# Kernel tuning notes

Measured on AMD Instinct MI355X. Metric: run time of the kernel, lower is better.

Reference implementation:

```python
import jax, jax.numpy as jnp
import numpy as np

B, T, D, H = 4, 2048, 1024, 16
DH = D // H


def setup_inputs() -> dict:
    key = jax.random.key(0)
    ks = jax.random.split(key, 7)
    s = 1.0 / np.sqrt(D)
    inp = {
        "query": jax.random.normal(ks[0], (B, T, D), jnp.float32),
        "key": jax.random.normal(ks[1], (B, T, D), jnp.float32),
        "value": jax.random.normal(ks[2], (B, T, D), jnp.float32),
        "wq": jax.random.normal(ks[3], (D, D), jnp.float32) * s,
        "wk": jax.random.normal(ks[4], (D, D), jnp.float32) * s,
        "wv": jax.random.normal(ks[5], (D, D), jnp.float32) * s,
        "wo": jax.random.normal(ks[6], (D, D), jnp.float32) * s,
    }
    # additive causal mask, broadcast over batch and heads
    neg = jnp.finfo(jnp.float32).min
    causal = jnp.where(jnp.tril(jnp.ones((T, T), bool)), 0.0, neg)
    inp["attn_mask"] = causal[None, None, :, :].astype(jnp.float32)
    return inp


def _split_heads(x):
    # [B, T, D] -> [B, H, T, DH]
    Bx, Tx, _ = x.shape
    return x.reshape(Bx, Tx, H, DH).transpose(0, 2, 1, 3)


def reference(query, key, value, attn_mask, wq, wk, wv, wo):
    # nn.Linear(bias=False): y = x @ W^T
    q = _split_heads(query @ wq.T)
    k = _split_heads(key @ wk.T)
    v = _split_heads(value @ wv.T)
    scale = 1.0 / jnp.sqrt(jnp.asarray(DH, q.dtype))
    scores = jnp.einsum("bhqd,bhkd->bhqk", q, k) * scale + attn_mask
    weights = jax.nn.softmax(scores, axis=-1)
    out = jnp.einsum("bhqk,bhkd->bhqd", weights, v)
    out = out.transpose(0, 2, 1, 3).reshape(query.shape[0], query.shape[1], D)
    out = out @ wo.T
    return out, k, v
```

## Files before the change

### kernel.cpp

```cpp
#include <hip/hip_runtime.h>
#include <hip/hip_bf16.h>
#include <math.h>

constexpr int Mdim = 8192;
constexpr int Ndim = 1024;
constexpr int Kdim = 1024;
constexpr int Tseq = 2048;
constexpr int NH   = 16;

typedef __attribute__((ext_vector_type(8))) short short8;
typedef __attribute__((ext_vector_type(4))) float floatx4;

__device__ __forceinline__ unsigned short f2b(float f) {
  unsigned int x = __builtin_bit_cast(unsigned int, f);
  x += 0x7fffu + ((x >> 16) & 1u);
  return (unsigned short)(x >> 16);
}
__device__ __forceinline__ unsigned int pk2(float a, float b) {
  unsigned int ua = __builtin_bit_cast(unsigned int, a) + 0x8000u;
  unsigned int ub = __builtin_bit_cast(unsigned int, b) + 0x8000u;
  return (ua >> 16) | (ub & 0xffff0000u);
}
__device__ __forceinline__ void gld16(const void* g, const void* l) {
  __builtin_amdgcn_global_load_lds(
      (const __attribute__((address_space(1))) unsigned int*)(unsigned long long)g,
      (__attribute__((address_space(3))) unsigned int*)(unsigned int)(unsigned long long)l,
      16, 0, 0);
}
__device__ __forceinline__ void barrier_raw() {
  __builtin_amdgcn_sched_barrier(0);
  __builtin_amdgcn_s_barrier();
  __builtin_amdgcn_sched_barrier(0);
}

__global__ __launch_bounds__(256) void cast_k(
    const float* __restrict__ q, const float* __restrict__ k,
    const float* __restrict__ v, const float* __restrict__ wq,
    const float* __restrict__ wk, const float* __restrict__ wv,
    const float* __restrict__ wo,
    unsigned short* d0, unsigned short* d1, unsigned short* d2,
    unsigned short* d3, unsigned short* d4, unsigned short* d5,
    unsigned short* d6) {
  int y = blockIdx.y;
  const float* s = y == 0 ? q : y == 1 ? k : y == 2 ? v
                 : y == 3 ? wq : y == 4 ? wk : y == 5 ? wv : wo;
  unsigned short* d = y == 0 ? d0 : y == 1 ? d1 : y == 2 ? d2
                    : y == 3 ? d3 : y == 4 ? d4 : y == 5 ? d5 : d6;
  size_t n = (y < 3) ? (size_t)Mdim * Kdim : (size_t)Ndim * Kdim;
  size_t i = ((size_t)blockIdx.x * 256 + threadIdx.x) * 8;
  if (i >= n) return;
  float4 a = *(const float4*)(s + i);
  float4 b = *(const float4*)(s + i + 4);
  uint4 w;
  w.x = (unsigned)f2b(a.x) | ((unsigned)f2b(a.y) << 16);
  w.y = (unsigned)f2b(a.z) | ((unsigned)f2b(a.w) << 16);
  w.z = (unsigned)f2b(b.x) | ((unsigned)f2b(b.y) << 16);
  w.w = (unsigned)f2b(b.z) | ((unsigned)f2b(b.w) << 16);
  *(uint4*)(d + i) = w;
}

__launch_bounds__(256, 4)
__global__ void gemm_qkv(const unsigned short* __restrict__ Aq,
                         const unsigned short* __restrict__ Ak,
                         const unsigned short* __restrict__ Av,
                         const unsigned short* __restrict__ Wq,
                         const unsigned short* __restrict__ Wk,
                         const unsigned short* __restrict__ Wv,
                         unsigned short* __restrict__ Qh,
                         unsigned short* __restrict__ Kh,
                         float* __restrict__ Kout,
                         unsigned short* __restrict__ VTg,
                         float* __restrict__ Vout) {
  __shared__ __align__(16) unsigned short As[128 * 64];
  __shared__ __align__(16) unsigned short Bs[128 * 64];

  const int flat = (blockIdx.z * 64 + blockIdx.y) * 8 + blockIdx.x;
  const int wgid = (flat & 7) * 192 + (flat >> 3);
  const int z    = wgid >> 9;
  const int rem  = wgid & 511;
  const int m0   = (rem >> 3) * 128;
  const int n0   = (rem & 7) * 128;

  const unsigned short* __restrict__ A = z == 0 ? Aq : z == 1 ? Ak : Av;
  const unsigned short* __restrict__ W = z == 0 ? Wq : z == 1 ? Wk : Wv;

  const int tid  = threadIdx.x;
  const int lane = tid & 63;
  const int wave = tid >> 6;
  const int l15  = lane & 15;
  const int quad = lane >> 4;
  const int sw   = l15 & 7;
  const int wm = (wave >> 1) * 64;
  const int wn = (wave & 1) * 64;

  floatx4 acc[4][4];
  for (int i = 0; i < 4; i++)
    for (int j = 0; j < 4; j++) acc[i][j] = (floatx4)0.0f;

  const int srow8 = lane >> 3;
  const int sg    = lane & 7;

  for (int kt = 0; kt < Kdim; kt += 64) {
    for (int jj = 0; jj < 4; jj++) {
      int cc = wave * 4 + jj;
      int row = cc * 8 + srow8;
      int G = sg ^ (row & 7);
      gld16(A + (size_t)(m0 + row) * Kdim + kt + G * 8, As + cc * 512);
      gld16(W + (size_t)(n0 + row) * Kdim + kt + G * 8, Bs + cc * 512);
    }
    __syncthreads();

    for (int hf = 0; hf < 2; hf++) {
      short8 af[4], bw[4];
      for (int mi = 0; mi < 4; mi++)
        af[mi] = *(const short8*)(As + (wm + mi * 16 + l15) * 64 +
                                  (((hf * 4 + quad) ^ sw) << 3));
      for (int ni = 0; ni < 4; ni++)
        bw[ni] = *(const short8*)(Bs + (wn + ni * 16 + l15) * 64 +
                                  (((hf * 4 + quad) ^ sw) << 3));
      for (int mi = 0; mi < 4; mi++)
        for (int ni = 0; ni < 4; ni++)
          acc[mi][ni] = __builtin_amdgcn_mfma_f32_16x16x32_bf16(
              bw[ni], af[mi], acc[mi][ni], 0, 0, 0);
    }
    __syncthreads();
  }

  const int gm = m0 + wm + l15;
  for (int mi = 0; mi < 4; mi++) {
    int t_abs = gm + mi * 16;
    int b = t_abs >> 11, tb = t_abs & (Tseq - 1);
    for (int ni = 0; ni < 4; ni++) {
      int gn0 = n0 + wn + ni * 16 + quad * 4;
      int h = gn0 >> 6, dh0 = gn0 & 63;
      size_t base = ((size_t)((b * NH + h) * Tseq + tb)) * 64 + dh0;
      floatx4 v = acc[mi][ni];
      if (z == 0) {
        ushort4 w = {f2b(v[0]), f2b(v[1]), f2b(v[2]), f2b(v[3])};
        *(ushort4*)(Qh + base) = w;
      } else if (z == 1) {
        *(float4*)(Kout + base) = *(float4*)&v;
        ushort4 w = {f2b(v[0]), f2b(v[1]), f2b(v[2]), f2b(v[3])};
        *(ushort4*)(Kh + base) = w;
      } else {
        *(float4*)(Vout + base) = *(float4*)&v;
        size_t vtb = ((size_t)((b * NH + h) * 64 + dh0)) * Tseq + tb;
        for (int r = 0; r < 4; r++)
          VTg[vtb + (size_t)r * Tseq] = f2b(v[r]);
      }
    }
  }
}

__launch_bounds__(256)
__global__ void gemm_o(const unsigned short* __restrict__ A,
                       const unsigned short* __restrict__ W,
                       float* __restrict__ Cf) {
  __shared__ __align__(16) unsigned short As[128 * 64];
  __shared__ __align__(16) unsigned short Bs[128 * 64];

  const int tid  = threadIdx.x;
  const int lane = tid & 63;
  const int wave = tid >> 6;
  const int l15  = lane & 15;
  const int quad = lane >> 4;
  const int sw   = l15 & 7;
  const int m0 = blockIdx.y * 128;
  const int n0 = blockIdx.x * 128;
  const int wm = (wave >> 1) * 64;
  const int wn = (wave & 1) * 64;

  floatx4 acc[4][4];
  for (int i = 0; i < 4; i++)
    for (int j = 0; j < 4; j++) acc[i][j] = (floatx4)0.0f;

  const int srow8 = lane >> 3;
  const int sg    = lane & 7;

  for (int kt = 0; kt < Kdim; kt += 64) {
    for (int jj = 0; jj < 4; jj++) {
      int cc = wave * 4 + jj;
      int row = cc * 8 + srow8;
      int G = sg ^ (row & 7);
      gld16(A + (size_t)(m0 + row) * Kdim + kt + G * 8, As + cc * 512);
      gld16(W + (size_t)(n0 + row) * Kdim + kt + G * 8, Bs + cc * 512);
    }
    __syncthreads();

    for (int hf = 0; hf < 2; hf++) {
      short8 af[4], bw[4];
      for (int mi = 0; mi < 4; mi++)
        af[mi] = *(const short8*)(As + (wm + mi * 16 + l15) * 64 +
                                  (((hf * 4 + quad) ^ sw) << 3));
      for (int ni = 0; ni < 4; ni++)
        bw[ni] = *(const short8*)(Bs + (wn + ni * 16 + l15) * 64 +
                                  (((hf * 4 + quad) ^ sw) << 3));
      for (int mi = 0; mi < 4; mi++)
        for (int ni = 0; ni < 4; ni++)
          acc[mi][ni] = __builtin_amdgcn_mfma_f32_16x16x32_bf16(
              bw[ni], af[mi], acc[mi][ni], 0, 0, 0);
    }
    __syncthreads();
  }

  for (int mi = 0; mi < 4; mi++) {
    int t_abs = m0 + wm + mi * 16 + l15;
    for (int ni = 0; ni < 4; ni++) {
      int gn0 = n0 + wn + ni * 16 + quad * 4;
      floatx4 v = acc[mi][ni];
      *(float4*)(Cf + (size_t)t_abs * Ndim + gn0) = *(float4*)&v;
    }
  }
}

__launch_bounds__(256)
__global__ void attn_k(const unsigned short* __restrict__ Qh,
                       const unsigned short* __restrict__ Kh,
                       const unsigned short* __restrict__ VTg,
                       unsigned short* __restrict__ Og) {
  __shared__ __align__(16) unsigned short Kt[2][64 * 64];
  __shared__ __align__(16) unsigned short Vt[2][64 * 64];
  __shared__ __align__(16) unsigned short Pl[64 * 64];

  const int tid  = threadIdx.x;
  const int lane = tid & 63;
  const int wave = tid >> 6;
  const int l15  = lane & 15;
  const int quad = lane >> 4;
  const int sw   = l15 & 7;
  const int bh   = blockIdx.x;

  const size_t headoff = (size_t)bh * Tseq * 64;
  const int srow8 = lane >> 3;
  const int sg    = lane & 7;
  const float kscale = 0.18033688011112042f;
  const int b = bh >> 4, h = bh & 15;

  for (int half = 0; half < 2; half++) {
    const int a   = half ? blockIdx.y : 31 - blockIdx.y;
    const int nkt = a + 1;
    const int qg  = a * 64 + wave * 16 + l15;

    short8 bq[2];
#pragma unroll
    for (int hf = 0; hf < 2; hf++)
      bq[hf] = *(const short8*)(Qh + headoff + (size_t)qg * 64 +
                                hf * 32 + quad * 8);

    floatx4 o[4];
#pragma unroll
    for (int nb = 0; nb < 4; nb++) o[nb] = (floatx4)0.0f;
    float mrow = -INFINITY, lrow = 0.0f;

    auto stage = [&](int par, int kt) {
      const int k0 = kt * 64;
#pragma unroll
      for (int jj = 0; jj < 2; jj++) {
        int cc  = wave * 2 + jj;
        int row = cc * 8 + srow8;
        int G   = sg ^ (row & 7);
        gld16(Kh + headoff + (size_t)(k0 + row) * 64 + G * 8,
              &Kt[par][cc * 512]);
        gld16(VTg + ((size_t)bh * 64 + row) * Tseq + k0 + G * 8,
              &Vt[par][cc * 512]);
      }
    };

    stage(0, 0);
    __builtin_amdgcn_sched_barrier(0);
    asm volatile("s_waitcnt vmcnt(0)");
    barrier_raw();

    for (int kt = 0; kt < nkt; kt++) {
      const int par = kt & 1;
      if (kt + 1 < nkt) stage(par ^ 1, kt + 1);
      const int k0 = kt * 64;

      floatx4 st[4];
#pragma unroll
      for (int nb = 0; nb < 4; nb++) {
        const unsigned short* kr = &Kt[par][(nb * 16 + l15) * 64];
        short8 ak0 = *(const short8*)(kr + ((quad ^ sw) << 3));
        short8 ak1 = *(const short8*)(kr + (((quad + 4) ^ sw) << 3));
        floatx4 acc0 = (floatx4)0.0f;
        acc0 = __builtin_amdgcn_mfma_f32_16x16x32_bf16(ak0, bq[0], acc0, 0, 0, 0);
        acc0 = __builtin_amdgcn_mfma_f32_16x16x32_bf16(ak1, bq[1], acc0, 0, 0, 0);
        st[nb] = acc0;
      }

      if (kt == nkt - 1) {
#pragma unroll
        for (int nb = 0; nb < 4; nb++)
#pragma unroll
          for (int r = 0; r < 4; r++) {
            int kg = k0 + nb * 16 + quad * 4 + r;
            if (kg > qg) st[nb][r] = -INFINITY;
          }
      }

      float mt = fmaxf(fmaxf(st[0][0], st[0][1]), fmaxf(st[0][2], st[0][3]));
#pragma unroll
      for (int nb = 1; nb < 4; nb++)
        mt = fmaxf(mt, fmaxf(fmaxf(st[nb][0], st[nb][1]),
                             fmaxf(st[nb][2], st[nb][3])));
      mt = fmaxf(mt, __shfl_xor(mt, 16, 64));
      mt = fmaxf(mt, __shfl_xor(mt, 32, 64));

      if (!__all((mt - mrow) * kscale <= 8.0f)) {
        float mnew = fmaxf(mrow, mt);
        float al = __builtin_amdgcn_exp2f((mrow - mnew) * kscale);
        mrow = mnew;
        lrow *= al;
#pragma unroll
        for (int nb = 0; nb < 4; nb++)
#pragma unroll
          for (int r = 0; r < 4; r++) o[nb][r] *= al;
      }
      const float ms = mrow * kscale;

      float rs = 0.0f;
      const int prow = (wave * 16 + l15) * 64;
#pragma unroll
      for (int nb = 0; nb < 4; nb++) {
        float p0 = __builtin_amdgcn_exp2f(__builtin_fmaf(st[nb][0], kscale, -ms));
        float p1 = __builtin_amdgcn_exp2f(__builtin_fmaf(st[nb][1], kscale, -ms));
        float p2 = __builtin_amdgcn_exp2f(__builtin_fmaf(st[nb][2], kscale, -ms));
        float p3 = __builtin_amdgcn_exp2f(__builtin_fmaf(st[nb][3], kscale, -ms));
        rs += (p0 + p1) + (p2 + p3);
        uint2 w = {pk2(p0, p1), pk2(p2, p3)};
        int klb = nb * 16 + quad * 4;
        int colp = (((klb >> 3) ^ sw) << 3) | (klb & 7);
        *(uint2*)(Pl + prow + colp) = w;
      }
      rs += __shfl_xor(rs, 16, 64);
      rs += __shfl_xor(rs, 32, 64);
      lrow += rs;

      short8 av[4][2];
#pragma unroll
      for (int nb = 0; nb < 4; nb++) {
        const unsigned short* vr = &Vt[par][(nb * 16 + l15) * 64];
        av[nb][0] = *(const short8*)(vr + ((quad ^ sw) << 3));
        av[nb][1] = *(const short8*)(vr + (((quad + 4) ^ sw) << 3));
      }
      const unsigned short* pr = Pl + prow;
      short8 bp0 = *(const short8*)(pr + ((quad ^ sw) << 3));
      short8 bp1 = *(const short8*)(pr + (((quad + 4) ^ sw) << 3));
#pragma unroll
      for (int nb = 0; nb < 4; nb++) {
        o[nb] = __builtin_amdgcn_mfma_f32_16x16x32_bf16(av[nb][0], bp0, o[nb], 0, 0, 0);
        o[nb] = __builtin_amdgcn_mfma_f32_16x16x32_bf16(av[nb][1], bp1, o[nb], 0, 0, 0);
      }

      __builtin_amdgcn_sched_barrier(0);
      asm volatile("s_waitcnt vmcnt(0)");
      barrier_raw();
    }

    float inv = 1.0f / lrow;
    size_t rowoff = ((size_t)(b * Tseq + qg)) * 1024 + h * 64;
#pragma unroll
    for (int nb = 0; nb < 4; nb++) {
      ushort4 w;
      w.x = f2b(o[nb][0] * inv);
      w.y = f2b(o[nb][1] * inv);
      w.z = f2b(o[nb][2] * inv);
      w.w = f2b(o[nb][3] * inv);
      *(ushort4*)(Og + rowoff + nb * 16 + quad * 4) = w;
    }
  }
}

extern "C" void kernel_launch(void* const* d_in, const int* in_sizes, int n_in,
                              void* d_out, int out_size, void* d_ws, size_t ws_size,
                              hipStream_t stream) {
  const float* q  = (const float*)d_in[0];
  const float* k  = (const float*)d_in[1];
  const float* v  = (const float*)d_in[2];
  const float* wq = (const float*)d_in[3];
  const float* wk = (const float*)d_in[4];
  const float* wv = (const float*)d_in[5];
  const float* wo = (const float*)d_in[6];
  float* out = (float*)d_out;

  constexpr size_t BTD = (size_t)Mdim * Kdim;
  constexpr size_t DD  = (size_t)Ndim * Kdim;
  constexpr size_t MB16 = BTD * 2;

  char* ws = (char*)d_ws;
  unsigned short* Qh  = (unsigned short*)(ws);
  unsigned short* Kh  = (unsigned short*)(ws + MB16);
  unsigned short* VTg = (unsigned short*)(ws + 2 * MB16);
  unsigned short* Og  = (unsigned short*)(ws + 3 * MB16);
  unsigned short* qb  = (unsigned short*)(ws + 4 * MB16);
  unsigned short* kb  = (unsigned short*)(ws + 5 * MB16);
  unsigned short* vb  = (unsigned short*)(ws + 6 * MB16);
  unsigned short* wqb = (unsigned short*)(ws + 7 * MB16);
  unsigned short* wkb = wqb + DD;
  unsigned short* wvb = wkb + DD;
  unsigned short* wob = wvb + DD;

  float* Kout = out + BTD;
  float* Vout = out + 2 * BTD;

  cast_k<<<dim3(4096, 7), 256, 0, stream>>>(q, k, v, wq, wk, wv, wo,
                                            qb, kb, vb, wqb, wkb, wvb, wob);

  gemm_qkv<<<dim3(8, 64, 3), 256, 0, stream>>>(
      qb, kb, vb, wqb, wkb, wvb, Qh, Kh, Kout, VTg, Vout);

  attn_k<<<dim3(4 * NH, 16), 256, 0, stream>>>(Qh, Kh, VTg, Og);

  gemm_o<<<dim3(Ndim / 128, Mdim / 128), 256, 0, stream>>>(Og, wob, out);
}
```

Measured before the change: 366.2 us.

## Retile output GEMM, split attention blocks per query tile, single-buffer V

The attention kernel now launches one block per 64-row query tile instead of pairing two tiles per block, and keeps only a single V buffer in shared memory. V is loaded in the same iteration it is used, with a mid-iteration wait before the PV product. Packed bf16 conversion and a three-input max instruction replace manual bit tricks and pairwise maxes. The output GEMM uses 64x128 tiles with a grouped block ordering and occupancy hints, which doubles the block count and shrinks shared memory per block. Together these aim to raise occupancy and parallelism, at the cost of losing the causal load balancing from pairing and exposing V load latency.

```diff
diff --git a/kernel.cpp b/kernel.cpp
--- a/kernel.cpp
+++ b/kernel.cpp
@@ -16,10 +16,15 @@
   x += 0x7fffu + ((x >> 16) & 1u);
   return (unsigned short)(x >> 16);
 }
-__device__ __forceinline__ unsigned int pk2(float a, float b) {
-  unsigned int ua = __builtin_bit_cast(unsigned int, a) + 0x8000u;
-  unsigned int ub = __builtin_bit_cast(unsigned int, b) + 0x8000u;
-  return (ua >> 16) | (ub & 0xffff0000u);
+__device__ __forceinline__ unsigned int cvtpk(float a, float b) {
+  unsigned int r;
+  asm("v_cvt_pk_bf16_f32 %0, %1, %2" : "=v"(r) : "v"(a), "v"(b));
+  return r;
+}
+__device__ __forceinline__ float max3f(float a, float b, float c) {
+  float d;
+  asm("v_max3_f32 %0, %1, %2, %3" : "=v"(d) : "v"(a), "v"(b), "v"(c));
+  return d;
 }
 __device__ __forceinline__ void gld16(const void* g, const void* l) {
   __builtin_amdgcn_global_load_lds(
@@ -152,12 +157,17 @@
   }
 }
 
-__launch_bounds__(256)
+__launch_bounds__(256, 6)
 __global__ void gemm_o(const unsigned short* __restrict__ A,
                        const unsigned short* __restrict__ W,
                        float* __restrict__ Cf) {
-  __shared__ __align__(16) unsigned short As[128 * 64];
+  __shared__ __align__(16) unsigned short As[64 * 64];
   __shared__ __align__(16) unsigned short Bs[128 * 64];
+
+  const int flat = blockIdx.y * 8 + blockIdx.x;
+  const int wgid = (flat & 7) * 128 + (flat >> 3);
+  const int m0   = (wgid >> 3) * 64;
+  const int n0   = (wgid & 7) * 128;
 
   const int tid  = threadIdx.x;
   const int lane = tid & 63;
@@ -165,37 +175,40 @@
   const int l15  = lane & 15;
   const int quad = lane >> 4;
   const int sw   = l15 & 7;
-  const int m0 = blockIdx.y * 128;
-  const int n0 = blockIdx.x * 128;
-  const int wm = (wave >> 1) * 64;
+  const int wm = (wave >> 1) * 32;
   const int wn = (wave & 1) * 64;
 
-  floatx4 acc[4][4];
-  for (int i = 0; i < 4; i++)
+  floatx4 acc[2][4];
+  for (int i = 0; i < 2; i++)
     for (int j = 0; j < 4; j++) acc[i][j] = (floatx4)0.0f;
 
   const int srow8 = lane >> 3;
   const int sg    = lane & 7;
 
   for (int kt = 0; kt < Kdim; kt += 64) {
+    for (int jj = 0; jj < 2; jj++) {
+      int cc = wave * 2 + jj;
+      int row = cc * 8 + srow8;
+      int G = sg ^ (row & 7);
+      gld16(A + (size_t)(m0 + row) * Kdim + kt + G * 8, As + cc * 512);
+    }
     for (int jj = 0; jj < 4; jj++) {
       int cc = wave * 4 + jj;
       int row = cc * 8 + srow8;
       int G = sg ^ (row & 7);
-      gld16(A + (size_t)(m0 + row) * Kdim + kt + G * 8, As + cc * 512);
       gld16(W + (size_t)(n0 + row) * Kdim + kt + G * 8, Bs + cc * 512);
     }
     __syncthreads();
 
     for (int hf = 0; hf < 2; hf++) {
-      short8 af[4], bw[4];
-      for (int mi = 0; mi < 4; mi++)
+      short8 af[2], bw[4];
+      for (int mi = 0; mi < 2; mi++)
         af[mi] = *(const short8*)(As + (wm + mi * 16 + l15) * 64 +
                                   (((hf * 4 + quad) ^ sw) << 3));
       for (int ni = 0; ni < 4; ni++)
         bw[ni] = *(const short8*)(Bs + (wn + ni * 16 + l15) * 64 +
                                   (((hf * 4 + quad) ^ sw) << 3));
-      for (int mi = 0; mi < 4; mi++)
+      for (int mi = 0; mi < 2; mi++)
         for (int ni = 0; ni < 4; ni++)
           acc[mi][ni] = __builtin_amdgcn_mfma_f32_16x16x32_bf16(
               bw[ni], af[mi], acc[mi][ni], 0, 0, 0);
@@ -203,7 +216,7 @@
     __syncthreads();
   }
 
-  for (int mi = 0; mi < 4; mi++) {
+  for (int mi = 0; mi < 2; mi++) {
     int t_abs = m0 + wm + mi * 16 + l15;
     for (int ni = 0; ni < 4; ni++) {
       int gn0 = n0 + wn + ni * 16 + quad * 4;
@@ -213,13 +226,13 @@
   }
 }
 
-__launch_bounds__(256)
+__launch_bounds__(256, 5)
 __global__ void attn_k(const unsigned short* __restrict__ Qh,
                        const unsigned short* __restrict__ Kh,
                        const unsigned short* __restrict__ VTg,
                        unsigned short* __restrict__ Og) {
   __shared__ __align__(16) unsigned short Kt[2][64 * 64];
-  __shared__ __align__(16) unsigned short Vt[2][64 * 64];
+  __shared__ __align__(16) unsigned short Vt[64 * 64];
   __shared__ __align__(16) unsigned short Pl[64 * 64];
 
   const int tid  = threadIdx.x;
@@ -229,145 +242,158 @@
   const int quad = lane >> 4;
   const int sw   = l15 & 7;
   const int bh   = blockIdx.x;
+  const int a    = 31 - (int)blockIdx.y;
+  const int nkt  = a + 1;
 
   const size_t headoff = (size_t)bh * Tseq * 64;
   const int srow8 = lane >> 3;
   const int sg    = lane & 7;
   const float kscale = 0.18033688011112042f;
   const int b = bh >> 4, h = bh & 15;
-
-  for (int half = 0; half < 2; half++) {
-    const int a   = half ? blockIdx.y : 31 - blockIdx.y;
-    const int nkt = a + 1;
-    const int qg  = a * 64 + wave * 16 + l15;
-
-    short8 bq[2];
-#pragma unroll
-    for (int hf = 0; hf < 2; hf++)
-      bq[hf] = *(const short8*)(Qh + headoff + (size_t)qg * 64 +
-                                hf * 32 + quad * 8);
-
-    floatx4 o[4];
-#pragma unroll
-    for (int nb = 0; nb < 4; nb++) o[nb] = (floatx4)0.0f;
-    float mrow = -INFINITY, lrow = 0.0f;
-
-    auto stage = [&](int par, int kt) {
-      const int k0 = kt * 64;
-#pragma unroll
-      for (int jj = 0; jj < 2; jj++) {
-        int cc  = wave * 2 + jj;
-        int row = cc * 8 + srow8;
-        int G   = sg ^ (row & 7);
-        gld16(Kh + headoff + (size_t)(k0 + row) * 64 + G * 8,
-              &Kt[par][cc * 512]);
-        gld16(VTg + ((size_t)bh * 64 + row) * Tseq + k0 + G * 8,
-              &Vt[par][cc * 512]);
-      }
-    };
-
-    stage(0, 0);
+  const int qg = a * 64 + wave * 16 + l15;
+
+  short8 bq[2];
+#pragma unroll
+  for (int hf = 0; hf < 2; hf++)
+    bq[hf] = *(const short8*)(Qh + headoff + (size_t)qg * 64 +
+                              hf * 32 + quad * 8);
+
+  floatx4 o[4];
+#pragma unroll
+  for (int nb = 0; nb < 4; nb++) o[nb] = (floatx4)0.0f;
+  float mrow = -INFINITY, lrow = 0.0f;
+
+  auto stageK = [&](int par, int kt) {
+    const int k0 = kt * 64;
+#pragma unroll
+    for (int jj = 0; jj < 2; jj++) {
+      int cc  = wave * 2 + jj;
+      int row = cc * 8 + srow8;
+      int G   = sg ^ (row & 7);
+      gld16(Kh + headoff + (size_t)(k0 + row) * 64 + G * 8, &Kt[par][cc * 512]);
+    }
+  };
+  auto stageV = [&](int kt) {
+    const int k0 = kt * 64;
+#pragma unroll
+    for (int jj = 0; jj < 2; jj++) {
+      int cc  = wave * 2 + jj;
+      int row = cc * 8 + srow8;
+      int G   = sg ^ (row & 7);
+      gld16(VTg + ((size_t)bh * 64 + row) * Tseq + k0 + G * 8, Vt + cc * 512);
+    }
+  };
+
+  stageK(0, 0);
+  __builtin_amdgcn_sched_barrier(0);
+  asm volatile("s_waitcnt vmcnt(0)");
+  barrier_raw();
+
+  for (int kt = 0; kt < nkt; kt++) {
+    const int par = kt & 1;
+    const int k0 = kt * 64;
+    stageV(kt);
+    const bool pre = (kt + 1 < nkt);
+    if (pre) stageK(par ^ 1, kt + 1);
+    __builtin_amdgcn_sched_barrier(0);
+
+    floatx4 st[4];
+#pragma unroll
+    for (int nb = 0; nb < 4; nb++) {
+      const unsigned short* kr = &Kt[par][(nb * 16 + l15) * 64];
+      short8 ak0 = *(const short8*)(kr + ((quad ^ sw) << 3));
+      short8 ak1 = *(const short8*)(kr + (((quad + 4) ^ sw) << 3));
+      floatx4 acc0 = (floatx4)0.0f;
+      acc0 = __builtin_amdgcn_mfma_f32_16x16x32_bf16(ak0, bq[0], acc0, 0, 0, 0);
+      acc0 = __builtin_amdgcn_mfma_f32_16x16x32_bf16(ak1, bq[1], acc0, 0, 0, 0);
+      st[nb] = acc0;
+    }
+
+    if (kt == nkt - 1) {
+#pragma unroll
+      for (int nb = 0; nb < 4; nb++)
+#pragma unroll
+        for (int r = 0; r < 4; r++) {
+          int kg = k0 + nb * 16 + quad * 4 + r;
+          if (kg > qg) st[nb][r] = -INFINITY;
+        }
+    }
+
+    float m0_ = max3f(st[0][0], st[0][1], st[0][2]);
+    float m1_ = max3f(st[0][3], st[1][0], st[1][1]);
+    float m2_ = max3f(st[1][2], st[1][3], st[2][0]);
+    float m3_ = max3f(st[2][1], st[2][2], st[2][3]);
+    float m4_ = max3f(st[3][0], st[3][1], st[3][2]);
+    float mt = fmaxf(max3f(m0_, m1_, m2_), max3f(m3_, m4_, st[3][3]));
+    mt = fmaxf(mt, __shfl_xor(mt, 16, 64));
+    mt = fmaxf(mt, __shfl_xor(mt, 32, 64));
+
+    if (!__all((mt - mrow) * kscale <= 8.0f)) {
+      float mnew = fmaxf(mrow, mt);
+      float al = __builtin_amdgcn_exp2f((mrow - mnew) * kscale);
+      mrow = mnew;
+      lrow *= al;
+#pragma unroll
+      for (int nb = 0; nb < 4; nb++)
+#pragma unroll
+        for (int r = 0; r < 4; r++) o[nb][r] *= al;
+    }
+    const float ms = mrow * kscale;
+
+    float rs = 0.0f;
+    const int prow = (wave * 16 + l15) * 64;
+#pragma unroll
+    for (int nb = 0; nb < 4; nb++) {
+      float p0 = __builtin_amdgcn_exp2f(__builtin_fmaf(st[nb][0], kscale, -ms));
+      float p1 = __builtin_amdgcn_exp2f(__builtin_fmaf(st[nb][1], kscale, -ms));
+      float p2 = __builtin_amdgcn_exp2f(__builtin_fmaf(st[nb][2], kscale, -ms));
+      float p3 = __builtin_amdgcn_exp2f(__builtin_fmaf(st[nb][3], kscale, -ms));
+      rs += (p0 + p1) + (p2 + p3);
+      uint2 w = {cvtpk(p0, p1), cvtpk(p2, p3)};
+      int klb = nb * 16 + quad * 4;
+      int colp = (((klb >> 3) ^ sw) << 3) | (klb & 7);
+      *(uint2*)(Pl + prow + colp) = w;
+    }
+    rs += __shfl_xor(rs, 16, 64);
+    rs += __shfl_xor(rs, 32, 64);
+    lrow += rs;
+
+    __builtin_amdgcn_sched_barrier(0);
+    if (pre) asm volatile("s_waitcnt vmcnt(2)");
+    else     asm volatile("s_waitcnt vmcnt(0)");
+    barrier_raw();
+
+    short8 av[4][2];
+#pragma unroll
+    for (int nb = 0; nb < 4; nb++) {
+      const unsigned short* vr = Vt + (nb * 16 + l15) * 64;
+      av[nb][0] = *(const short8*)(vr + ((quad ^ sw) << 3));
+      av[nb][1] = *(const short8*)(vr + (((quad + 4) ^ sw) << 3));
+    }
+    const unsigned short* pr = Pl + prow;
+    short8 bp0 = *(const short8*)(pr + ((quad ^ sw) << 3));
+    short8 bp1 = *(const short8*)(pr + (((quad + 4) ^ sw) << 3));
+#pragma unroll
+    for (int nb = 0; nb < 4; nb++) {
+      o[nb] = __builtin_amdgcn_mfma_f32_16x16x32_bf16(av[nb][0], bp0, o[nb], 0, 0, 0);
+      o[nb] = __builtin_amdgcn_mfma_f32_16x16x32_bf16(av[nb][1], bp1, o[nb], 0, 0, 0);
+    }
+
     __builtin_amdgcn_sched_barrier(0);
     asm volatile("s_waitcnt vmcnt(0)");
     barrier_raw();
-
-    for (int kt = 0; kt < nkt; kt++) {
-      const int par = kt & 1;
-      if (kt + 1 < nkt) stage(par ^ 1, kt + 1);
-      const int k0 = kt * 64;
-
-      floatx4 st[4];
-#pragma unroll
-      for (int nb = 0; nb < 4; nb++) {
-        const unsigned short* kr = &Kt[par][(nb * 16 + l15) * 64];
-        short8 ak0 = *(const short8*)(kr + ((quad ^ sw) << 3));
-        short8 ak1 = *(const short8*)(kr + (((quad + 4) ^ sw) << 3));
-        floatx4 acc0 = (floatx4)0.0f;
-        acc0 = __builtin_amdgcn_mfma_f32_16x16x32_bf16(ak0, bq[0], acc0, 0, 0, 0);
-        acc0 = __builtin_amdgcn_mfma_f32_16x16x32_bf16(ak1, bq[1], acc0, 0, 0, 0);
-        st[nb] = acc0;
-      }
-
-      if (kt == nkt - 1) {
-#pragma unroll
-        for (int nb = 0; nb < 4; nb++)
-#pragma unroll
-          for (int r = 0; r < 4; r++) {
-            int kg = k0 + nb * 16 + quad * 4 + r;
-            if (kg > qg) st[nb][r] = -INFINITY;
-          }
-      }
-
-      float mt = fmaxf(fmaxf(st[0][0], st[0][1]), fmaxf(st[0][2], st[0][3]));
-#pragma unroll
-      for (int nb = 1; nb < 4; nb++)
-        mt = fmaxf(mt, fmaxf(fmaxf(st[nb][0], st[nb][1]),
-                             fmaxf(st[nb][2], st[nb][3])));
-      mt = fmaxf(mt, __shfl_xor(mt, 16, 64));
-      mt = fmaxf(mt, __shfl_xor(mt, 32, 64));
-
-      if (!__all((mt - mrow) * kscale <= 8.0f)) {
-        float mnew = fmaxf(mrow, mt);
-        float al = __builtin_amdgcn_exp2f((mrow - mnew) * kscale);
-        mrow = mnew;
-        lrow *= al;
-#pragma unroll
-        for (int nb = 0; nb < 4; nb++)
-#pragma unroll
-          for (int r = 0; r < 4; r++) o[nb][r] *= al;
-      }
-      const float ms = mrow * kscale;
-
-      float rs = 0.0f;
-      const int prow = (wave * 16 + l15) * 64;
-#pragma unroll
-      for (int nb = 0; nb < 4; nb++) {
-        float p0 = __builtin_amdgcn_exp2f(__builtin_fmaf(st[nb][0], kscale, -ms));
-        float p1 = __builtin_amdgcn_exp2f(__builtin_fmaf(st[nb][1], kscale, -ms));
-        float p2 = __builtin_amdgcn_exp2f(__builtin_fmaf(st[nb][2], kscale, -ms));
-        float p3 = __builtin_amdgcn_exp2f(__builtin_fmaf(st[nb][3], kscale, -ms));
-        rs += (p0 + p1) + (p2 + p3);
-        uint2 w = {pk2(p0, p1), pk2(p2, p3)};
-        int klb = nb * 16 + quad * 4;
-        int colp = (((klb >> 3) ^ sw) << 3) | (klb & 7);
-        *(uint2*)(Pl + prow + colp) = w;
-      }
-      rs += __shfl_xor(rs, 16, 64);
-      rs += __shfl_xor(rs, 32, 64);
-      lrow += rs;
-
-      short8 av[4][2];
-#pragma unroll
-      for (int nb = 0; nb < 4; nb++) {
-        const unsigned short* vr = &Vt[par][(nb * 16 + l15) * 64];
-        av[nb][0] = *(const short8*)(vr + ((quad ^ sw) << 3));
-        av[nb][1] = *(const short8*)(vr + (((quad + 4) ^ sw) << 3));
-      }
-      const unsigned short* pr = Pl + prow;
-      short8 bp0 = *(const short8*)(pr + ((quad ^ sw) << 3));
-      short8 bp1 = *(const short8*)(pr + (((quad + 4) ^ sw) << 3));
-#pragma unroll
-      for (int nb = 0; nb < 4; nb++) {
-        o[nb] = __builtin_amdgcn_mfma_f32_16x16x32_bf16(av[nb][0], bp0, o[nb], 0, 0, 0);
-        o[nb] = __builtin_amdgcn_mfma_f32_16x16x32_bf16(av[nb][1], bp1, o[nb], 0, 0, 0);
-      }
-
-      __builtin_amdgcn_sched_barrier(0);
-      asm volatile("s_waitcnt vmcnt(0)");
-      barrier_raw();
-    }
-
-    float inv = 1.0f / lrow;
-    size_t rowoff = ((size_t)(b * Tseq + qg)) * 1024 + h * 64;
-#pragma unroll
-    for (int nb = 0; nb < 4; nb++) {
-      ushort4 w;
-      w.x = f2b(o[nb][0] * inv);
-      w.y = f2b(o[nb][1] * inv);
-      w.z = f2b(o[nb][2] * inv);
-      w.w = f2b(o[nb][3] * inv);
-      *(ushort4*)(Og + rowoff + nb * 16 + quad * 4) = w;
-    }
+  }
+
+  float inv = 1.0f / lrow;
+  size_t rowoff = ((size_t)(b * Tseq + qg)) * 1024 + h * 64;
+#pragma unroll
+  for (int nb = 0; nb < 4; nb++) {
+    ushort4 w;
+    w.x = f2b(o[nb][0] * inv);
+    w.y = f2b(o[nb][1] * inv);
+    w.z = f2b(o[nb][2] * inv);
+    w.w = f2b(o[nb][3] * inv);
+    *(ushort4*)(Og + rowoff + nb * 16 + quad * 4) = w;
   }
 }
 
@@ -409,7 +435,7 @@
   gemm_qkv<<<dim3(8, 64, 3), 256, 0, stream>>>(
       qb, kb, vb, wqb, wkb, wvb, Qh, Kh, Kout, VTg, Vout);
 
-  attn_k<<<dim3(4 * NH, 16), 256, 0, stream>>>(Qh, Kh, VTg, Og);
-
-  gemm_o<<<dim3(Ndim / 128, Mdim / 128), 256, 0, stream>>>(Og, wob, out);
-}
+  attn_k<<<dim3(4 * NH, 32), 256, 0, stream>>>(Qh, Kh, VTg, Og);
+
+  gemm_o<<<dim3(8, Mdim / 64), 256, 0, stream>>>(Og, wob, out);
+}
```

New measurement: 385.0 us. 1.05x slower.
